# Kernel optimization log

Measured on AMD Instinct MI355X. Metric: run time of the kernel, lower is better.

The kernel has to match this reference:

```python
import jax, jax.numpy as jnp
import numpy as np

EMBED = 1024
HEADS = 16
HEAD_DIM = EMBED // HEADS


def setup_inputs() -> dict:
    key = jax.random.key(0)
    ks = jax.random.split(key, 10)
    s = 1.0 / np.sqrt(EMBED)
    inp = {
        "x": jax.random.normal(ks[0], (4, 2048, EMBED), dtype=jnp.float32),
        "mask": jax.random.randint(ks[1], (4, 2048), 0, 2, dtype=jnp.int32),
        "Wq": jax.random.uniform(ks[2], (EMBED, EMBED), jnp.float32, -s, s),
        "bq": jax.random.uniform(ks[3], (EMBED,), jnp.float32, -s, s),
        "Wk": jax.random.uniform(ks[4], (EMBED, EMBED), jnp.float32, -s, s),
        "bk": jax.random.uniform(ks[5], (EMBED,), jnp.float32, -s, s),
        "Wv": jax.random.uniform(ks[6], (EMBED, EMBED), jnp.float32, -s, s),
        "bv": jax.random.uniform(ks[7], (EMBED,), jnp.float32, -s, s),
        "Wo": jax.random.uniform(ks[8], (EMBED, EMBED), jnp.float32, -s, s),
        "bo": jax.random.uniform(ks[9], (EMBED,), jnp.float32, -s, s),
    }
    return inp


def reference(x, mask, Wq, bq, Wk, bk, Wv, bv, Wo, bo):
    B, S, E = x.shape
    scale = np.sqrt(HEAD_DIM).astype(np.float32)

    def split_heads(t):  # [B,S,E] -> [B,H,S,D]
        return t.reshape(B, S, HEADS, HEAD_DIM).transpose(0, 2, 1, 3)

    Q = split_heads(x @ Wq.T + bq)
    K = split_heads(x @ Wk.T + bk)
    V = split_heads(x @ Wv.T + bv)

    scores = jnp.einsum("bhqd,bhkd->bhqk", Q, K) / scale  # [B,H,S,S]
    # mask [B,S] broadcast over heads and query dim (key-padding mask)
    scores = jnp.where(mask[:, None, None, :] == 0, -jnp.inf, scores)
    weights = jax.nn.softmax(scores, axis=-1)
    out = jnp.einsum("bhqk,bhkd->bhqd", weights, V)  # [B,H,S,D]
    out = out.transpose(0, 2, 1, 3).reshape(B, S, E)
    return out @ Wo.T + bo
```

## Files before the change

kernel.cpp:

```cpp
#include <hip/hip_runtime.h>

#define BATCH 4
#define SEQ   2048
#define EMBED 1024
#define HEADS 16
#define HDIM  64
#define NTOK  (BATCH*SEQ)

typedef __attribute__((ext_vector_type(8)))  short short8;
typedef __attribute__((ext_vector_type(4)))  float f32x4;
typedef __attribute__((ext_vector_type(16))) float f32x16;

static __device__ __forceinline__ unsigned short f2bf(float f) {
    union { float f; unsigned u; } v; v.f = f;
    return (unsigned short)((v.u + 0x7FFFu + ((v.u >> 16) & 1u)) >> 16);
}
static __device__ __forceinline__ unsigned cvtpk(float lo, float hi) {
    unsigned r;
    asm("v_cvt_pk_bf16_f32 %0, %1, %2" : "=v"(r) : "v"(lo), "v"(hi));
    return r;
}
static __device__ __forceinline__ void gload_lds16(const unsigned short* g, unsigned short* l) {
    __builtin_amdgcn_global_load_lds(
        (__attribute__((address_space(1))) void*)g,
        (__attribute__((address_space(3))) void*)l, 16, 0, 0);
}

#define SCQ 0.180336880f

__global__ void cast_all(const float* __restrict__ x,
                         const float* __restrict__ w0, const float* __restrict__ w1,
                         const float* __restrict__ w2, const float* __restrict__ w3,
                         unsigned short* __restrict__ xb,
                         unsigned short* __restrict__ wb)
{
    const int bid = blockIdx.x;
    const float* src;
    unsigned short* dst;
    int i;
    if (bid < 4096) {
        src = x; dst = xb; i = (bid * 256 + threadIdx.x) * 8;
    } else {
        const int wz = (bid - 4096) >> 9;
        const float* ws[4] = {w0, w1, w2, w3};
        src = ws[wz];
        dst = wb + (size_t)wz * (EMBED * EMBED);
        i = (((bid - 4096) & 511) * 256 + threadIdx.x) * 8;
    }
    float4 a = *(const float4*)(src + i);
    float4 b = *(const float4*)(src + i + 4);
    union { int4 v; unsigned short u[8]; } pk;
    pk.u[0] = f2bf(a.x); pk.u[1] = f2bf(a.y); pk.u[2] = f2bf(a.z); pk.u[3] = f2bf(a.w);
    pk.u[4] = f2bf(b.x); pk.u[5] = f2bf(b.y); pk.u[6] = f2bf(b.z); pk.u[7] = f2bf(b.w);
    *(int4*)(dst + i) = pk.v;
}

__global__ __launch_bounds__(256, 2)
void gemm_qkv(const unsigned short* __restrict__ Xb,
              const unsigned short* __restrict__ Wall,
              const float* __restrict__ bq, const float* __restrict__ bk,
              const float* __restrict__ bv,
              unsigned short* __restrict__ Qw, unsigned short* __restrict__ Kw,
              unsigned short* __restrict__ VtG)
{
    __shared__ unsigned short Ws[2][3][128][32];
    __shared__ unsigned short Xs[2][128][32];

    const int tid  = threadIdx.x;
    const int bx   = blockIdx.x, by = blockIdx.y;
    const int f0   = (by >> 3) * 128;
    const int t0   = ((bx << 3) | (by & 7)) * 128;
    const int lane = tid & 63, m = lane & 15, quad = lane >> 4;
    const int wid  = tid >> 6;
    const int wf   = (wid & 1) * 64;
    const int wt   = (wid >> 1) * 64;

    const int r    = tid >> 2, cc = tid & 3, sw = (tid >> 4) & 3;
    const int gcol = (cc ^ sw) << 3;
    const unsigned short* Xp = Xb + (size_t)(t0 + r) * EMBED + gcol;
    const unsigned short* Wp = Wall + (size_t)(f0 + r) * EMBED + gcol;
    unsigned short* XsL[2] = { &Xs[0][0][0] + tid * 8, &Xs[1][0][0] + tid * 8 };
    unsigned short* WsL[2] = { &Ws[0][0][0][0] + tid * 8, &Ws[1][0][0][0] + tid * 8 };

    const int qs = (quad ^ ((m >> 2) & 3)) << 3;

    f32x4 aq[4][4] = {}, ak[4][4] = {}, av[4][4] = {};

    for (int k0 = 0; k0 < EMBED; k0 += 64) {
        __syncthreads();
#pragma unroll
        for (int hf = 0; hf < 2; ++hf) {
            const int kk = k0 + hf * 32;
            gload_lds16(Xp + kk,              XsL[hf]);
            gload_lds16(Xp + kk + 64 * EMBED, XsL[hf] + 2048);
#pragma unroll
            for (int z = 0; z < 3; ++z) {
                const unsigned short* wz = Wp + (size_t)z * EMBED * EMBED + kk;
                gload_lds16(wz,              WsL[hf] + z * 4096);
                gload_lds16(wz + 64 * EMBED, WsL[hf] + z * 4096 + 2048);
            }
        }
        __syncthreads();

#pragma unroll
        for (int hf = 0; hf < 2; ++hf) {
            short8 bf4[4];
#pragma unroll
            for (int nb = 0; nb < 4; ++nb)
                bf4[nb] = *(const short8*)&Xs[hf][wt + nb * 16 + m][qs];

#pragma unroll
            for (int z = 0; z < 3; ++z) {
                short8 af[4];
#pragma unroll
                for (int mb = 0; mb < 4; ++mb)
                    af[mb] = *(const short8*)&Ws[hf][z][wf + mb * 16 + m][qs];
                f32x4 (&acc)[4][4] = (z == 0) ? aq : (z == 1) ? ak : av;
#pragma unroll
                for (int mb = 0; mb < 4; ++mb)
#pragma unroll
                    for (int nb = 0; nb < 4; ++nb)
                        acc[mb][nb] = __builtin_amdgcn_mfma_f32_16x16x32_bf16(
                            af[mb], bf4[nb], acc[mb][nb], 0, 0, 0);
            }
        }
    }

#pragma unroll
    for (int mb = 0; mb < 4; ++mb) {
        const int feat = f0 + wf + mb * 16 + quad * 4;
        float4 bv4 = *(const float4*)&bq[feat];
#pragma unroll
        for (int nb = 0; nb < 4; ++nb) {
            const int tok = t0 + wt + nb * 16 + m;
            ushort4 pk;
            pk.x = f2bf((aq[mb][nb][0] + bv4.x) * SCQ);
            pk.y = f2bf((aq[mb][nb][1] + bv4.y) * SCQ);
            pk.z = f2bf((aq[mb][nb][2] + bv4.z) * SCQ);
            pk.w = f2bf((aq[mb][nb][3] + bv4.w) * SCQ);
            *(ushort4*)(Qw + (size_t)tok * EMBED + feat) = pk;
        }
    }
#pragma unroll
    for (int mb = 0; mb < 4; ++mb) {
        const int feat = f0 + wf + mb * 16 + quad * 4;
        float4 bv4 = *(const float4*)&bk[feat];
#pragma unroll
        for (int nb = 0; nb < 4; ++nb) {
            const int tok = t0 + wt + nb * 16 + m;
            ushort4 pk;
            pk.x = f2bf(ak[mb][nb][0] + bv4.x);
            pk.y = f2bf(ak[mb][nb][1] + bv4.y);
            pk.z = f2bf(ak[mb][nb][2] + bv4.z);
            pk.w = f2bf(ak[mb][nb][3] + bv4.w);
            *(ushort4*)(Kw + (size_t)tok * EMBED + feat) = pk;
        }
    }
    {
        const int h = (f0 + wf) >> 6;
#pragma unroll
        for (int nb = 0; nb < 4; ++nb) {
            const int tok = t0 + wt + nb * 16 + m;
            const int b   = tok >> 11;
            const int s   = tok & (SEQ - 1);
            const int sp  = (s & ~12) | ((s & 4) << 1) | ((s & 8) >> 1);
            const size_t base = ((size_t)(b * HEADS + h) * HDIM) * SEQ + sp;
#pragma unroll
            for (int mb = 0; mb < 4; ++mb) {
                const int feat  = f0 + wf + mb * 16 + quad * 4;
                const int dbase = mb * 16 + quad * 4;
                float4 bv4 = *(const float4*)&bv[feat];
                VtG[base + (size_t)(dbase + 0) * SEQ] = f2bf(av[mb][nb][0] + bv4.x);
                VtG[base + (size_t)(dbase + 1) * SEQ] = f2bf(av[mb][nb][1] + bv4.y);
                VtG[base + (size_t)(dbase + 2) * SEQ] = f2bf(av[mb][nb][2] + bv4.z);
                VtG[base + (size_t)(dbase + 3) * SEQ] = f2bf(av[mb][nb][3] + bv4.w);
            }
        }
    }
}

__global__ __launch_bounds__(256, 4)
void attn_mfma(const unsigned short* __restrict__ Qb,
               const unsigned short* __restrict__ Kb,
               const unsigned short* __restrict__ VtG,
               const int* __restrict__ mask,
               unsigned short* __restrict__ Ob)
{
    __shared__ unsigned short Ks[2][64][72];
    __shared__ unsigned short Vs[2][64][72];

    const int tid  = threadIdx.x;
    const int lin  = (blockIdx.x & 7) * 128 + (blockIdx.x >> 3);
    const int qb   = lin & 15;
    const int h    = (lin >> 4) & 15;
    const int b    = lin >> 8;
    const int wid  = tid >> 6, lane = tid & 63;
    const int q32  = lane & 31, hi = lane >> 5;
    const int tb   = b * SEQ;
    const int q    = qb * 128 + wid * 32 + q32;

    const unsigned short* qrow = Qb + (size_t)(tb + q) * EMBED + h * HDIM;
    short8 qf[4];
#pragma unroll
    for (int st = 0; st < 4; ++st)
        qf[st] = *(const short8*)(qrow + st * 16 + hi * 8);

    const int* mrow = mask + b * SEQ;
    unsigned long long mbits = 0;
#pragma unroll 8
    for (int j = 0; j < 64; ++j)
        mbits |= (unsigned long long)(mrow[j * 32 + q32] != 0 ? 1 : 0) << j;

    short8 mqf = {0, 0, 0, 0, 0, 0, 0, 0};
    mqf[0] = hi ? (short)0 : (short)0xC480;

    f32x16 o0, o1, z16;
#pragma unroll
    for (int i = 0; i < 16; ++i) { z16[i] = 0.f; }
    o0 = z16; o1 = z16;
    float lr = 0.f;

    const int sr = tid >> 2, sc = (tid & 3) * 16;
    const unsigned short* kSrc = Kb + (size_t)(tb + sr) * EMBED + h * HDIM + sc;
    const unsigned short* vSrc = VtG + ((size_t)(b * HEADS + h) * HDIM + sr) * SEQ + sc;

    auto compute = [&](const unsigned short (*Kc)[72],
                       const unsigned short (*Vc)[72], int jb) {
        __builtin_amdgcn_s_setprio(1);
        short8 mkfa = {0, 0, 0, 0, 0, 0, 0, 0};
        short8 mkfb = {0, 0, 0, 0, 0, 0, 0, 0};
        mkfa[0] = (hi == 0 && !((mbits >> jb) & 1))       ? (short)0x3F80 : (short)0;
        mkfb[0] = (hi == 0 && !((mbits >> (jb + 1)) & 1)) ? (short)0x3F80 : (short)0;

        f32x16 s[2];
        s[0] = __builtin_amdgcn_mfma_f32_32x32x16_bf16(mkfa, mqf, z16, 0, 0, 0);
        s[1] = __builtin_amdgcn_mfma_f32_32x32x16_bf16(mkfb, mqf, z16, 0, 0, 0);
#pragma unroll
        for (int kb = 0; kb < 2; ++kb)
#pragma unroll
            for (int st = 0; st < 4; ++st) {
                short8 kf = *(const short8*)&Kc[kb * 32 + q32][st * 16 + hi * 8];
                s[kb] = __builtin_amdgcn_mfma_f32_32x32x16_bf16(kf, qf[st], s[kb], 0, 0, 0);
            }

#pragma unroll
        for (int kb = 0; kb < 2; ++kb) {
            float p[16];
#pragma unroll
            for (int i = 0; i < 16; ++i) p[i] = __builtin_amdgcn_exp2f(s[kb][i]);

            lr += (((p[0] + p[1]) + (p[2] + p[3])) + ((p[4] + p[5]) + (p[6] + p[7])))
                + (((p[8] + p[9]) + (p[10] + p[11])) + ((p[12] + p[13]) + (p[14] + p[15])));

            unsigned D[8];
#pragma unroll
            for (int j = 0; j < 8; ++j) D[j] = cvtpk(p[2 * j], p[2 * j + 1]);

#pragma unroll
            for (int cl = 0; cl < 2; ++cl) {
                union { uint4 u; short8 s8; } fr;
                fr.u.x = D[4 * cl + 0]; fr.u.y = D[4 * cl + 1];
                fr.u.z = D[4 * cl + 2]; fr.u.w = D[4 * cl + 3];

                const int kcol = kb * 32 + cl * 16 + hi * 8;
                short8 vf0 = *(const short8*)&Vc[q32][kcol];
                short8 vf1 = *(const short8*)&Vc[32 + q32][kcol];
                o0 = __builtin_amdgcn_mfma_f32_32x32x16_bf16(vf0, fr.s8, o0, 0, 0, 0);
                o1 = __builtin_amdgcn_mfma_f32_32x32x16_bf16(vf1, fr.s8, o1, 0, 0, 0);
            }
        }
        __builtin_amdgcn_s_setprio(0);
    };

    {
        int4 kv0 = *(const int4*)(kSrc);
        int4 kv1 = *(const int4*)(kSrc + 8);
        int4 vv0 = *(const int4*)(vSrc);
        int4 vv1 = *(const int4*)(vSrc + 8);
        *(int4*)&Ks[0][sr][sc]     = kv0;
        *(int4*)&Ks[0][sr][sc + 8] = kv1;
        *(int4*)&Vs[0][sr][sc]     = vv0;
        *(int4*)&Vs[0][sr][sc + 8] = vv1;
        __syncthreads();
    }

    int cur = 0;
    for (int kt = 0; kt + 64 < SEQ; kt += 64) {
        const unsigned short* kp = kSrc + (size_t)(kt + 64) * EMBED;
        int4 kv0 = *(const int4*)(kp);
        int4 kv1 = *(const int4*)(kp + 8);
        int4 vv0 = *(const int4*)(vSrc + kt + 64);
        int4 vv1 = *(const int4*)(vSrc + kt + 64 + 8);

        compute(Ks[cur], Vs[cur], kt >> 5);

        __syncthreads();
        const int nxt = cur ^ 1;
        *(int4*)&Ks[nxt][sr][sc]     = kv0;
        *(int4*)&Ks[nxt][sr][sc + 8] = kv1;
        *(int4*)&Vs[nxt][sr][sc]     = vv0;
        *(int4*)&Vs[nxt][sr][sc + 8] = vv1;
        __syncthreads();
        cur = nxt;
    }
    compute(Ks[cur], Vs[cur], (SEQ - 64) >> 5);

    const float lrt = lr + __shfl_xor(lr, 32);
    const float inv = 1.0f / lrt;
    unsigned short* orow = Ob + (size_t)(tb + q) * EMBED + h * HDIM;
#pragma unroll
    for (int db = 0; db < 2; ++db) {
        const f32x16& oo = db ? o1 : o0;
#pragma unroll
        for (int qg = 0; qg < 4; ++qg) {
            ushort4 pk;
            pk.x = f2bf(oo[qg * 4 + 0] * inv);
            pk.y = f2bf(oo[qg * 4 + 1] * inv);
            pk.z = f2bf(oo[qg * 4 + 2] * inv);
            pk.w = f2bf(oo[qg * 4 + 3] * inv);
            *(ushort4*)(orow + db * 32 + qg * 8 + hi * 4) = pk;
        }
    }
}

__global__ __launch_bounds__(256, 2)
void gemm_o(const unsigned short* __restrict__ W, const unsigned short* __restrict__ X,
            const float* __restrict__ bias, float* __restrict__ Cout)
{
    __shared__ unsigned short Ws[2][128][32];
    __shared__ unsigned short Xs[2][128][32];

    const int tid  = threadIdx.x;
    const int bx   = blockIdx.x, by = blockIdx.y;
    const int f0   = (by >> 3) * 128;
    const int t0   = ((bx << 3) | (by & 7)) * 128;
    const int lane = tid & 63, m = lane & 15, quad = lane >> 4;
    const int wid  = tid >> 6;
    const int wf   = (wid & 1) * 64;
    const int wt   = (wid >> 1) * 64;

    const int r    = tid >> 2, cc = tid & 3, sw = (tid >> 4) & 3;
    const int gcol = (cc ^ sw) << 3;
    const unsigned short* Wp = W + (size_t)(f0 + r) * EMBED + gcol;
    const unsigned short* Xp = X + (size_t)(t0 + r) * EMBED + gcol;
    unsigned short* WsL[2] = { &Ws[0][0][0] + tid * 8, &Ws[1][0][0] + tid * 8 };
    unsigned short* XsL[2] = { &Xs[0][0][0] + tid * 8, &Xs[1][0][0] + tid * 8 };

    const int qs = (quad ^ ((m >> 2) & 3)) << 3;

    f32x4 acc[4][4] = {};

    for (int k0 = 0; k0 < EMBED; k0 += 64) {
        __syncthreads();
#pragma unroll
        for (int hf = 0; hf < 2; ++hf) {
            const int kk = k0 + hf * 32;
            gload_lds16(Wp + kk,              WsL[hf]);
            gload_lds16(Wp + kk + 64 * EMBED, WsL[hf] + 2048);
            gload_lds16(Xp + kk,              XsL[hf]);
            gload_lds16(Xp + kk + 64 * EMBED, XsL[hf] + 2048);
        }
        __syncthreads();

#pragma unroll
        for (int hf = 0; hf < 2; ++hf) {
            short8 af[4], bf4[4];
#pragma unroll
            for (int mb = 0; mb < 4; ++mb)
                af[mb] = *(const short8*)&Ws[hf][wf + mb * 16 + m][qs];
#pragma unroll
            for (int nb = 0; nb < 4; ++nb)
                bf4[nb] = *(const short8*)&Xs[hf][wt + nb * 16 + m][qs];
#pragma unroll
            for (int mb = 0; mb < 4; ++mb)
#pragma unroll
                for (int nb = 0; nb < 4; ++nb)
                    acc[mb][nb] = __builtin_amdgcn_mfma_f32_16x16x32_bf16(
                        af[mb], bf4[nb], acc[mb][nb], 0, 0, 0);
        }
    }

#pragma unroll
    for (int mb = 0; mb < 4; ++mb) {
        const int feat = f0 + wf + mb * 16 + quad * 4;
        float4 bv4 = *(const float4*)&bias[feat];
#pragma unroll
        for (int nb = 0; nb < 4; ++nb) {
            const int tok = t0 + wt + nb * 16 + m;
            float4 st;
            st.x = acc[mb][nb][0] + bv4.x;
            st.y = acc[mb][nb][1] + bv4.y;
            st.z = acc[mb][nb][2] + bv4.z;
            st.w = acc[mb][nb][3] + bv4.w;
            *(float4*)(Cout + (size_t)tok * EMBED + feat) = st;
        }
    }
}

extern "C" void kernel_launch(void* const* d_in, const int* in_sizes, int n_in,
                              void* d_out, int out_size, void* d_ws, size_t ws_size,
                              hipStream_t stream)
{
    const float* x    = (const float*)d_in[0];
    const int*   mask = (const int*)  d_in[1];
    const float* Wq   = (const float*)d_in[2];
    const float* bq   = (const float*)d_in[3];
    const float* Wk   = (const float*)d_in[4];
    const float* bk   = (const float*)d_in[5];
    const float* Wv   = (const float*)d_in[6];
    const float* bv   = (const float*)d_in[7];
    const float* Wo   = (const float*)d_in[8];
    const float* bo   = (const float*)d_in[9];
    float* out = (float*)d_out;

    const size_t NE = (size_t)NTOK * EMBED;
    const size_t WE = (size_t)EMBED * EMBED;
    unsigned short* Xb  = (unsigned short*)d_ws;
    unsigned short* Wqb = Xb + NE;
    unsigned short* Wob = Wqb + 3 * WE;
    unsigned short* Qw  = Wob + WE;
    unsigned short* Kw  = Qw + NE;
    unsigned short* VtG = Kw + NE;
    unsigned short* Ow  = Xb;

    cast_all<<<4096 + 2048, 256, 0, stream>>>(x, Wq, Wk, Wv, Wo, Xb, Wqb);

    gemm_qkv<<<dim3(8, 64), 256, 0, stream>>>(Xb, Wqb, bq, bk, bv, Qw, Kw, VtG);

    attn_mfma<<<BATCH * HEADS * (SEQ / 128), 256, 0, stream>>>(Qw, Kw, VtG, mask, Ow);

    gemm_o<<<dim3(8, 64), 256, 0, stream>>>(Wob, Ow, bo, out);
}
```

Before: 263.8 us.

## Double-buffer LDS loads to overlap global fetch with MFMA in projection GEMMs

The QKV and output projection GEMMs previously loaded a full 64-wide K slab into both LDS halves and only then computed, with two barriers per iteration. Now the two halves act as a ping-pong buffer. The next 32-wide K slice is issued with global_load_lds while the MFMAs run on the current one, and there is a single barrier per step. This hides global-load latency behind compute, but doubles the number of loop iterations and barriers per K, and correctness relies on the barrier waiting for the async LDS loads.

```diff
diff --git a/kernel.cpp b/kernel.cpp
--- a/kernel.cpp
+++ b/kernel.cpp
@@ -86,45 +86,47 @@
 
     f32x4 aq[4][4] = {}, ak[4][4] = {}, av[4][4] = {};
 
-    for (int k0 = 0; k0 < EMBED; k0 += 64) {
+    auto stage = [&](int kk, int bf) {
+        gload_lds16(Xp + kk,              XsL[bf]);
+        gload_lds16(Xp + kk + 64 * EMBED, XsL[bf] + 2048);
+#pragma unroll
+        for (int z = 0; z < 3; ++z) {
+            const unsigned short* wz = Wp + (size_t)z * EMBED * EMBED + kk;
+            gload_lds16(wz,              WsL[bf] + z * 4096);
+            gload_lds16(wz + 64 * EMBED, WsL[bf] + z * 4096 + 2048);
+        }
+    };
+    auto step = [&](int bf) {
+        short8 bf4[4];
+#pragma unroll
+        for (int nb = 0; nb < 4; ++nb)
+            bf4[nb] = *(const short8*)&Xs[bf][wt + nb * 16 + m][qs];
+#pragma unroll
+        for (int z = 0; z < 3; ++z) {
+            short8 af[4];
+#pragma unroll
+            for (int mb = 0; mb < 4; ++mb)
+                af[mb] = *(const short8*)&Ws[bf][z][wf + mb * 16 + m][qs];
+            f32x4 (&acc)[4][4] = (z == 0) ? aq : (z == 1) ? ak : av;
+#pragma unroll
+            for (int mb = 0; mb < 4; ++mb)
+#pragma unroll
+                for (int nb = 0; nb < 4; ++nb)
+                    acc[mb][nb] = __builtin_amdgcn_mfma_f32_16x16x32_bf16(
+                        af[mb], bf4[nb], acc[mb][nb], 0, 0, 0);
+        }
+    };
+
+    stage(0, 0);
+    __syncthreads();
+    int cur = 0;
+    for (int k0 = 0; k0 < EMBED - 32; k0 += 32) {
+        stage(k0 + 32, cur ^ 1);
+        step(cur);
         __syncthreads();
-#pragma unroll
-        for (int hf = 0; hf < 2; ++hf) {
-            const int kk = k0 + hf * 32;
-            gload_lds16(Xp + kk,              XsL[hf]);
-            gload_lds16(Xp + kk + 64 * EMBED, XsL[hf] + 2048);
-#pragma unroll
-            for (int z = 0; z < 3; ++z) {
-                const unsigned short* wz = Wp + (size_t)z * EMBED * EMBED + kk;
-                gload_lds16(wz,              WsL[hf] + z * 4096);
-                gload_lds16(wz + 64 * EMBED, WsL[hf] + z * 4096 + 2048);
-            }
-        }
-        __syncthreads();
-
-#pragma unroll
-        for (int hf = 0; hf < 2; ++hf) {
-            short8 bf4[4];
-#pragma unroll
-            for (int nb = 0; nb < 4; ++nb)
-                bf4[nb] = *(const short8*)&Xs[hf][wt + nb * 16 + m][qs];
-
-#pragma unroll
-            for (int z = 0; z < 3; ++z) {
-                short8 af[4];
-#pragma unroll
-                for (int mb = 0; mb < 4; ++mb)
-                    af[mb] = *(const short8*)&Ws[hf][z][wf + mb * 16 + m][qs];
-                f32x4 (&acc)[4][4] = (z == 0) ? aq : (z == 1) ? ak : av;
-#pragma unroll
-                for (int mb = 0; mb < 4; ++mb)
-#pragma unroll
-                    for (int nb = 0; nb < 4; ++nb)
-                        acc[mb][nb] = __builtin_amdgcn_mfma_f32_16x16x32_bf16(
-                            af[mb], bf4[nb], acc[mb][nb], 0, 0, 0);
-            }
-        }
-    }
+        cur ^= 1;
+    }
+    step(cur);
 
 #pragma unroll
     for (int mb = 0; mb < 4; ++mb) {
@@ -350,35 +352,38 @@
 
     f32x4 acc[4][4] = {};
 
-    for (int k0 = 0; k0 < EMBED; k0 += 64) {
+    auto stage = [&](int kk, int bf) {
+        gload_lds16(Wp + kk,              WsL[bf]);
+        gload_lds16(Wp + kk + 64 * EMBED, WsL[bf] + 2048);
+        gload_lds16(Xp + kk,              XsL[bf]);
+        gload_lds16(Xp + kk + 64 * EMBED, XsL[bf] + 2048);
+    };
+    auto step = [&](int bf) {
+        short8 af[4], bf4[4];
+#pragma unroll
+        for (int mb = 0; mb < 4; ++mb)
+            af[mb] = *(const short8*)&Ws[bf][wf + mb * 16 + m][qs];
+#pragma unroll
+        for (int nb = 0; nb < 4; ++nb)
+            bf4[nb] = *(const short8*)&Xs[bf][wt + nb * 16 + m][qs];
+#pragma unroll
+        for (int mb = 0; mb < 4; ++mb)
+#pragma unroll
+            for (int nb = 0; nb < 4; ++nb)
+                acc[mb][nb] = __builtin_amdgcn_mfma_f32_16x16x32_bf16(
+                    af[mb], bf4[nb], acc[mb][nb], 0, 0, 0);
+    };
+
+    stage(0, 0);
+    __syncthreads();
+    int cur = 0;
+    for (int k0 = 0; k0 < EMBED - 32; k0 += 32) {
+        stage(k0 + 32, cur ^ 1);
+        step(cur);
         __syncthreads();
-#pragma unroll
-        for (int hf = 0; hf < 2; ++hf) {
-            const int kk = k0 + hf * 32;
-            gload_lds16(Wp + kk,              WsL[hf]);
-            gload_lds16(Wp + kk + 64 * EMBED, WsL[hf] + 2048);
-            gload_lds16(Xp + kk,              XsL[hf]);
-            gload_lds16(Xp + kk + 64 * EMBED, XsL[hf] + 2048);
-        }
-        __syncthreads();
-
-#pragma unroll
-        for (int hf = 0; hf < 2; ++hf) {
-            short8 af[4], bf4[4];
-#pragma unroll
-            for (int mb = 0; mb < 4; ++mb)
-                af[mb] = *(const short8*)&Ws[hf][wf + mb * 16 + m][qs];
-#pragma unroll
-            for (int nb = 0; nb < 4; ++nb)
-                bf4[nb] = *(const short8*)&Xs[hf][wt + nb * 16 + m][qs];
-#pragma unroll
-            for (int mb = 0; mb < 4; ++mb)
-#pragma unroll
-                for (int nb = 0; nb < 4; ++nb)
-                    acc[mb][nb] = __builtin_amdgcn_mfma_f32_16x16x32_bf16(
-                        af[mb], bf4[nb], acc[mb][nb], 0, 0, 0);
-        }
-    }
+        cur ^= 1;
+    }
+    step(cur);
 
 #pragma unroll
     for (int mb = 0; mb < 4; ++mb) {
```

Result: slower. 272.7 us (+3.4%).
